# Kernel tuning notes

Hardware: AMD Instinct MI355X
Metric: run time of the kernel (lower is better)

The kernel has to match this reference:

```python
import jax, jax.numpy as jnp
import numpy as np

B, S, H, KVH, D = 2, 4096, 32, 8, 64
HID = H * D          # 2048
WIN = 256            # sliding window size (incl. self)
CHK = 128            # chunk size for linear attention
NREP = H // KVH


def setup_inputs() -> dict:
    key = jax.random.key(0)
    ks = jax.random.split(key, 5)
    hidden_states = jax.random.normal(ks[0], (B, S, HID), jnp.float32)
    # RoPE tables (Llama-style)
    inv_freq = 1.0 / (10000.0 ** (jnp.arange(0, D, 2, dtype=jnp.float32) / D))
    freqs = jnp.arange(S, dtype=jnp.float32)[:, None] * inv_freq[None, :]
    emb = jnp.concatenate([freqs, freqs], axis=-1)          # [S, D]
    cos = jnp.broadcast_to(jnp.cos(emb)[None], (B, S, D)).astype(jnp.float32)
    sin = jnp.broadcast_to(jnp.sin(emb)[None], (B, S, D)).astype(jnp.float32)
    scale = 0.02
    Wq = jax.random.normal(ks[1], (HID, HID), jnp.float32) * scale
    Wk = jax.random.normal(ks[2], (KVH * D, HID), jnp.float32) * scale
    Wv = jax.random.normal(ks[3], (KVH * D, HID), jnp.float32) * scale
    Wo = jax.random.normal(ks[4], (HID, HID), jnp.float32) * scale
    return {"hidden_states": hidden_states, "cos": cos, "sin": sin,
            "Wq": Wq, "Wk": Wk, "Wv": Wv, "Wo": Wo}


def rotate_half(x):
    x1, x2 = jnp.split(x, 2, axis=-1)
    return jnp.concatenate([-x2, x1], axis=-1)


def local_window_attention(q, k, v):
    nb = S // WIN
    qb = q.reshape(B, H, nb, WIN, D)
    kb = k.reshape(B, H, nb, WIN, D)
    vb = v.reshape(B, H, nb, WIN, D)
    zpad = jnp.zeros_like(kb[:, :, :1])
    kcat = jnp.concatenate([jnp.concatenate([zpad, kb[:, :, :-1]], axis=2), kb], axis=3)  # [B,H,nb,2W,D]
    vcat = jnp.concatenate([jnp.concatenate([zpad, vb[:, :, :-1]], axis=2), vb], axis=3)
    scores = jnp.einsum('bhnqd,bhnkd->bhnqk', qb, kcat) / jnp.sqrt(jnp.float32(D))
    i = jnp.arange(WIN)[:, None]          # query pos within block
    j = jnp.arange(2 * WIN)[None, :]      # key pos within concat window
    diff = i + WIN - j                    # q_abs - key_abs
    base = (diff >= 0) & (diff < WIN)     # causal + window
    n = jnp.arange(nb)[:, None, None]
    valid = (n * WIN + j[None] - WIN) >= 0   # key_abs >= 0 (mask block-0 padding)
    mask = base[None] & valid                # [nb, W, 2W]
    scores = jnp.where(mask[None, None], scores, -1e30)
    attn = jax.nn.softmax(scores, axis=-1)
    out = jnp.einsum('bhnqk,bhnkd->bhnqd', attn, vcat)
    return out.reshape(B, H, S, D)


def linear_memory_attention(q, k, v):
    # causal linear attention with elu+1 feature map, chunked prefix state
    phi = lambda x: jax.nn.elu(x) + 1.0
    nc = S // CHK
    pq = phi(q).reshape(B, H, nc, CHK, D)
    pk = phi(k).reshape(B, H, nc, CHK, D)
    vc = v.reshape(B, H, nc, CHK, D)
    # intra-chunk (causal within chunk)
    cm = jnp.tril(jnp.ones((CHK, CHK), bool))
    scores = jnp.einsum('bhncd,bhnkd->bhnck', pq, pk)
    scores = jnp.where(cm, scores, 0.0)
    num = jnp.einsum('bhnck,bhnkd->bhncd', scores, vc)
    den = scores.sum(-1)
    # inter-chunk via exclusive prefix sums of KV state
    kv = jnp.einsum('bhnkd,bhnke->bhnde', pk, vc)      # [B,H,nc,D,D]
    ks = pk.sum(axis=3)                                # [B,H,nc,D]
    z4 = jnp.zeros_like(kv[:, :, :1])
    Sprev = jnp.concatenate([z4, jnp.cumsum(kv, axis=2)[:, :, :-1]], axis=2)
    z3 = jnp.zeros_like(ks[:, :, :1])
    zprev = jnp.concatenate([z3, jnp.cumsum(ks, axis=2)[:, :, :-1]], axis=2)
    num = num + jnp.einsum('bhncd,bhnde->bhnce', pq, Sprev)
    den = den + jnp.einsum('bhncd,bhnd->bhnc', pq, zprev)
    out = num / (den[..., None] + 1e-6)
    return out.reshape(B, H, S, D)


def reference(hidden_states, cos, sin, Wq, Wk, Wv, Wo):
    q = jnp.einsum('bsh,oh->bso', hidden_states, Wq).reshape(B, S, H, D).transpose(0, 2, 1, 3)
    k = jnp.einsum('bsh,oh->bso', hidden_states, Wk).reshape(B, S, KVH, D).transpose(0, 2, 1, 3)
    v = jnp.einsum('bsh,oh->bso', hidden_states, Wv).reshape(B, S, KVH, D).transpose(0, 2, 1, 3)
    c = cos[:, None]  # [B,1,S,D]
    s = sin[:, None]
    q = q * c + rotate_half(q) * s
    k = k * c + rotate_half(k) * s
    k = jnp.repeat(k, NREP, axis=1)
    v = jnp.repeat(v, NREP, axis=1)
    local_out = local_window_attention(q, k, v)
    linear_out = linear_memory_attention(q, k, v)
    hybrid = 0.5 * local_out + 0.5 * linear_out              # [B,H,S,D]
    hybrid = hybrid.transpose(0, 2, 1, 3).reshape(B, S, HID)
    return jnp.einsum('bsh,oh->bso', hybrid, Wo)
```

## Files before the change

### kernel.cpp

```cpp
#include <hip/hip_runtime.h>

#define gB 2
#define gS 4096
#define gH 32
#define gKVH 8
#define gHID 2048
#define gNC 32
#define gBS (gB*gS)

using bf16x8 = __attribute__((ext_vector_type(8))) short;
using f32x4  = __attribute__((ext_vector_type(4))) float;

__device__ __forceinline__ float bf2f(unsigned short u){
  return __uint_as_float(((unsigned)u) << 16);
}
__device__ __forceinline__ unsigned short f2bf(float f){
  unsigned u = __float_as_uint(f);
  u = (u + 0x7fffu + ((u >> 16) & 1u)) >> 16;
  return (unsigned short)u;
}
__device__ __forceinline__ float phi_f(float x){ return x > 0.f ? x + 1.f : __expf(x); }

__device__ __forceinline__ void unpack8(uint4 v, unsigned short* o){
  o[0]=(unsigned short)(v.x&0xffffu); o[1]=(unsigned short)(v.x>>16);
  o[2]=(unsigned short)(v.y&0xffffu); o[3]=(unsigned short)(v.y>>16);
  o[4]=(unsigned short)(v.z&0xffffu); o[5]=(unsigned short)(v.z>>16);
  o[6]=(unsigned short)(v.w&0xffffu); o[7]=(unsigned short)(v.w>>16);
}
__device__ __forceinline__ uint4 pack8(const unsigned short* s){
  uint4 v;
  v.x = (unsigned)s[0] | ((unsigned)s[1]<<16);
  v.y = (unsigned)s[2] | ((unsigned)s[3]<<16);
  v.z = (unsigned)s[4] | ((unsigned)s[5]<<16);
  v.w = (unsigned)s[6] | ((unsigned)s[7]<<16);
  return v;
}

typedef const __attribute__((address_space(1))) void* gas_ptr;
typedef __attribute__((address_space(3))) void* las_ptr;
__device__ __forceinline__ void gload16(const void* g, void* l){
  __builtin_amdgcn_global_load_lds((gas_ptr)g, (las_ptr)l, 16, 0, 0);
}

__global__ void cvt_all(const float* __restrict__ hidden, const float* __restrict__ Wq,
                        const float* __restrict__ Wk, const float* __restrict__ Wv,
                        const float* __restrict__ Wo, unsigned short* __restrict__ hbf,
                        unsigned short* __restrict__ wqkv, unsigned short* __restrict__ wob)
{
  const long HG = (long)gBS*gHID/4;
  const long QG = 1048576, KG = 262144, VG = 262144, OG = 1048576;
  const long total = HG + QG + KG + VG + OG;
  long stride = (long)gridDim.x * blockDim.x;
  for (long i = (long)blockIdx.x*blockDim.x + threadIdx.x; i < total; i += stride){
    const float* src; unsigned short* dst; long off;
    if (i < HG)                { src = hidden; dst = hbf;                          off = i; }
    else if (i < HG+QG)        { src = Wq;     dst = wqkv;                         off = i - HG; }
    else if (i < HG+QG+KG)     { src = Wk;     dst = wqkv + (size_t)2048*gHID;     off = i - HG - QG; }
    else if (i < HG+QG+KG+VG)  { src = Wv;     dst = wqkv + (size_t)2560*gHID;     off = i - HG - QG - KG; }
    else                       { src = Wo;     dst = wob;                          off = i - HG - QG - KG - VG; }
    float4 v = *(const float4*)(src + off*4);
    ushort4 o;
    o.x = f2bf(v.x); o.y = f2bf(v.y); o.z = f2bf(v.z); o.w = f2bf(v.w);
    *(ushort4*)(dst + off*4) = o;
  }
}

__global__ __launch_bounds__(512, 2) void gemm_qkv(const unsigned short* __restrict__ A,
                                                   const unsigned short* __restrict__ Bm,
                                                   const float* __restrict__ cosb,
                                                   const float* __restrict__ sinb,
                                                   unsigned short* __restrict__ q_r,
                                                   unsigned short* __restrict__ k_r,
                                                   unsigned short* __restrict__ vproj)
{
  const int Kdim = 2048;
  __shared__ unsigned short Sh[2*24576];
  int tid = threadIdx.x, lane = tid & 63, w = tid >> 6, lr = lane & 15, lg = lane >> 4;
  int wm = w >> 2, wn = w & 3;
  const int ntn = 12;
  int nwg = gridDim.x;
  int bid = (int)blockIdx.x;
  int swz = (bid & 7) * (nwg >> 3) + (bid >> 3);
  long m0 = (long)(swz / ntn) * 128;
  long n0 = (long)(swz % ntn) * 256;
  const int NT = Kdim >> 6;

  f32x4 acc[4][4] = {};

  auto stage = [&](int t){
    int sbase = (t & 1) * 24576;
    int k0 = t << 6;
    #pragma unroll
    for (int i = 0; i < 2; ++i){
      int c = w*64 + lane + i*512;
      int row = c >> 3, g = c & 7;
      int colb = (g ^ (row & 7)) << 4;
      gload16((const char*)A + ((m0 + row) * (long)Kdim + k0) * 2 + colb,
              (void*)&Sh[sbase + (w*64 + i*512)*8]);
    }
    #pragma unroll
    for (int i = 0; i < 4; ++i){
      int c = w*64 + lane + i*512;
      int row = c >> 3, g = c & 7;
      int colb = (g ^ (row & 7)) << 4;
      gload16((const char*)Bm + ((n0 + row) * (long)Kdim + k0) * 2 + colb,
              (void*)&Sh[sbase + 8192 + (w*64 + i*512)*8]);
    }
  };

  stage(0);
  for (int t = 0; t < NT; ++t){
    asm volatile("s_waitcnt vmcnt(0)" ::: "memory");
    __builtin_amdgcn_s_barrier();
    if (t + 1 < NT) stage(t + 1);
    int sb = (t & 1) * 24576;
    #pragma unroll
    for (int kk = 0; kk < 2; ++kk){
      bf16x8 af[4], bfr[4];
      #pragma unroll
      for (int m = 0; m < 4; ++m){
        int row = wm*64 + m*16 + lr;
        af[m] = *(const bf16x8*)&Sh[sb + row*64 + (((kk*4 + lg) ^ (row & 7)) << 3)];
      }
      #pragma unroll
      for (int n = 0; n < 4; ++n){
        int row = wn*64 + n*16 + lr;
        bfr[n] = *(const bf16x8*)&Sh[sb + 8192 + row*64 + (((kk*4 + lg) ^ (row & 7)) << 3)];
      }
      __builtin_amdgcn_s_setprio(1);
      #pragma unroll
      for (int m = 0; m < 4; ++m)
        #pragma unroll
        for (int n = 0; n < 4; ++n)
          acc[m][n] = __builtin_amdgcn_mfma_f32_16x16x32_bf16(af[m], bfr[n], acc[m][n], 0, 0, 0);
      __builtin_amdgcn_s_setprio(0);
    }
  }

  long colbase = n0 + wn*64;
  if (colbase < 2048){
    int head = (int)(colbase >> 6);
    #pragma unroll
    for (int m = 0; m < 4; ++m)
      #pragma unroll
      for (int r = 0; r < 4; ++r){
        long srow = m0 + wm*64 + m*16 + 4*lg + r;
        int b = (int)(srow >> 12), s = (int)(srow & 4095);
        const float* cp = cosb + srow*64;
        const float* sp = sinb + srow*64;
        unsigned short* op = q_r + ((size_t)(b*gH + head)*gS + s)*64;
        #pragma unroll
        for (int n = 0; n < 2; ++n){
          int d = n*16 + lr;
          float x1 = acc[m][n][r], x2 = acc[m][n+2][r];
          op[d]      = f2bf(x1*cp[d]    - x2*sp[d]);
          op[d+32]   = f2bf(x2*cp[d+32] + x1*sp[d+32]);
        }
      }
  } else if (colbase < 2560){
    int head = (int)(colbase >> 6) - 32;
    #pragma unroll
    for (int m = 0; m < 4; ++m)
      #pragma unroll
      for (int r = 0; r < 4; ++r){
        long srow = m0 + wm*64 + m*16 + 4*lg + r;
        int b = (int)(srow >> 12), s = (int)(srow & 4095);
        const float* cp = cosb + srow*64;
        const float* sp = sinb + srow*64;
        unsigned short* op = k_r + ((size_t)(b*gKVH + head)*gS + s)*64;
        #pragma unroll
        for (int n = 0; n < 2; ++n){
          int d = n*16 + lr;
          float x1 = acc[m][n][r], x2 = acc[m][n+2][r];
          op[d]      = f2bf(x1*cp[d]    - x2*sp[d]);
          op[d+32]   = f2bf(x2*cp[d+32] + x1*sp[d+32]);
        }
      }
  } else {
    #pragma unroll
    for (int m = 0; m < 4; ++m)
      #pragma unroll
      for (int r = 0; r < 4; ++r){
        long srow = m0 + wm*64 + m*16 + 4*lg + r;
        unsigned short* op = vproj + (size_t)srow*512 + (colbase - 2560);
        #pragma unroll
        for (int n = 0; n < 4; ++n)
          op[n*16 + lr] = f2bf(acc[m][n][r]);
      }
  }
}

template<int OUT_BF16>
__global__ __launch_bounds__(512, 2) void gemm256(const unsigned short* __restrict__ A,
                                                  const unsigned short* __restrict__ Bm,
                                                  void* __restrict__ Cout,
                                                  int Mdim, int Ndim, int Kdim)
{
  __shared__ unsigned short Sh[2*32768];
  int tid = threadIdx.x, lane = tid & 63, w = tid >> 6, lr = lane & 15, lg = lane >> 4;
  int wm = w >> 2, wn = w & 3;
  int ntn = Ndim >> 8;
  int nwg = gridDim.x;
  int bid = (int)blockIdx.x;
  int swz = (bid & 7) * (nwg >> 3) + (bid >> 3);
  long m0 = (long)(swz / ntn) * 256;
  long n0 = (long)(swz % ntn) * 256;
  int NT = Kdim >> 6;

  f32x4 acc[8][4] = {};

  auto stage = [&](int t){
    int sbase = (t & 1) * 32768;
    int k0 = t << 6;
    #pragma unroll
    for (int i = 0; i < 4; ++i){
      int c = w*64 + lane + i*512;
      int row = c >> 3, g = c & 7;
      int colb = (g ^ (row & 7)) << 4;
      gload16((const char*)A + ((m0 + row) * (long)Kdim + k0) * 2 + colb,
              (void*)&Sh[sbase + (w*64 + i*512)*8]);
      gload16((const char*)Bm + ((n0 + row) * (long)Kdim + k0) * 2 + colb,
              (void*)&Sh[sbase + 16384 + (w*64 + i*512)*8]);
    }
  };

  stage(0);
  for (int t = 0; t < NT; ++t){
    asm volatile("s_waitcnt vmcnt(0)" ::: "memory");
    __builtin_amdgcn_s_barrier();
    if (t + 1 < NT) stage(t + 1);
    int sb = (t & 1) * 32768;
    #pragma unroll
    for (int kk = 0; kk < 2; ++kk){
      bf16x8 af[8], bfr[4];
      #pragma unroll
      for (int m = 0; m < 8; ++m){
        int row = wm*128 + m*16 + lr;
        af[m] = *(const bf16x8*)&Sh[sb + row*64 + (((kk*4 + lg) ^ (row & 7)) << 3)];
      }
      #pragma unroll
      for (int n = 0; n < 4; ++n){
        int row = wn*64 + n*16 + lr;
        bfr[n] = *(const bf16x8*)&Sh[sb + 16384 + row*64 + (((kk*4 + lg) ^ (row & 7)) << 3)];
      }
      __builtin_amdgcn_s_setprio(1);
      #pragma unroll
      for (int m = 0; m < 8; ++m)
        #pragma unroll
        for (int n = 0; n < 4; ++n)
          acc[m][n] = __builtin_amdgcn_mfma_f32_16x16x32_bf16(af[m], bfr[n], acc[m][n], 0, 0, 0);
      __builtin_amdgcn_s_setprio(0);
    }
  }

  #pragma unroll
  for (int m = 0; m < 8; ++m)
    #pragma unroll
    for (int n = 0; n < 4; ++n)
      #pragma unroll
      for (int r = 0; r < 4; ++r){
        long row = m0 + wm*128 + m*16 + 4*lg + r;
        long col = n0 + wn*64 + n*16 + lr;
        float v = acc[m][n][r];
        if (OUT_BF16) ((unsigned short*)Cout)[row*Ndim + col] = f2bf(v);
        else          ((float*)Cout)[row*Ndim + col] = v;
      }
}

__global__ __launch_bounds__(256) void transpose64(const unsigned short* __restrict__ in,
                                                   unsigned short* __restrict__ out,
                                                   int tokStride, int voff, int mode)
{
  __shared__ unsigned short T[64*72];
  int bid = blockIdx.x;
  int st = bid & 63; int kvh = (bid >> 6) & 7; int b = bid >> 9;
  int s0 = st*64;
  int tid = threadIdx.x;
  const unsigned short* ip;
  size_t tokstr;
  if (mode == 0){ ip = in + ((size_t)(b*gKVH+kvh)*gS + s0)*64;                  tokstr = 64; }
  else          { ip = in + (size_t)(b*gS+s0)*tokStride + voff + kvh*64;        tokstr = tokStride; }
  #pragma unroll
  for (int i = 0; i < 2; ++i){
    int cc = tid + 256*i; int sl = cc >> 3, ch = cc & 7;
    *(uint4*)&T[sl*72 + ch*8] = *(const uint4*)&ip[(size_t)sl*tokstr + ch*8];
  }
  __syncthreads();
  unsigned short* op = out + ((size_t)(b*gKVH+kvh)*64)*gS;
  #pragma unroll
  for (int i = 0; i < 2; ++i){
    int cc = tid + 256*i; int d = cc >> 3, ch = cc & 7;
    unsigned short t[8];
    #pragma unroll
    for (int u = 0; u < 8; ++u) t[u] = T[(ch*8+u)*72 + d];
    *(uint4*)&op[(size_t)d*gS + s0 + ch*8] = pack8(t);
  }
}

__global__ __launch_bounds__(512) void local_attn(const unsigned short* __restrict__ q_r,
                                                  const unsigned short* __restrict__ k_r,
                                                  const unsigned short* __restrict__ vt,
                                                  unsigned short* __restrict__ olocal)
{
  __shared__ unsigned short Qs[128*72];
  __shared__ unsigned short Ks[2][64*72];
  __shared__ unsigned short VTs[2][64*72];
  __shared__ unsigned short Ps[8*16*72];
  int bid = blockIdx.x;
  int qt = bid & 31; int h = (bid >> 5) & 31; int b = bid >> 10;
  int kvh = h >> 2;
  int q0 = qt*128;
  int tid = threadIdx.x, lane = tid & 63, w = tid >> 6, lr = lane & 15, lg = lane >> 4;
  const unsigned short* qp = q_r + ((size_t)(b*gH  +h  )*gS + q0)*64;
  const unsigned short* kp = k_r + ((size_t)(b*gKVH+kvh)*gS)*64;
  const unsigned short* vp = vt  + ((size_t)(b*gKVH+kvh)*64)*gS;

  #pragma unroll
  for (int i = 0; i < 2; ++i){
    int cc = tid + 512*i; int row = cc >> 3, ch = cc & 7;
    *(uint4*)&Qs[row*72 + ch*8] = *(const uint4*)&qp[row*64 + ch*8];
  }

  int kt0 = (q0 >= 256) ? 0 : ((256 - q0) >> 6);
  int krow = tid >> 3, kch = tid & 7;
  uint4 kreg, vreg;
  {
    int kb = q0 - 256 + kt0*64;
    kreg = *(const uint4*)&kp[(size_t)(kb+krow)*64 + kch*8];
    vreg = *(const uint4*)&vp[(size_t)krow*gS + kb + kch*8];
    *(uint4*)&Ks[0][krow*72 + kch*8]  = kreg;
    *(uint4*)&VTs[0][krow*72 + kch*8] = vreg;
  }

  float psum[4] = {0.f, 0.f, 0.f, 0.f};
  f32x4 accO[4] = {};
  int wq = w*16;

  for (int kt = kt0; kt < 6; ++kt){
    int cur = (kt - kt0) & 1;
    __syncthreads();
    bool more = (kt + 1 < 6);
    if (more){
      int kb2 = q0 - 256 + (kt+1)*64;
      kreg = *(const uint4*)&kp[(size_t)(kb2+krow)*64 + kch*8];
      vreg = *(const uint4*)&vp[(size_t)krow*gS + kb2 + kch*8];
    }

    f32x4 sc[4] = {};
    #pragma unroll
    for (int kk = 0; kk < 64; kk += 32){
      bf16x8 aq = *(const bf16x8*)&Qs[(wq+lr)*72 + kk + 8*lg];
      #pragma unroll
      for (int f = 0; f < 4; ++f){
        bf16x8 bk = *(const bf16x8*)&Ks[cur][(f*16+lr)*72 + kk + 8*lg];
        sc[f] = __builtin_amdgcn_mfma_f32_16x16x32_bf16(aq, bk, sc[f], 0, 0, 0);
      }
    }
    #pragma unroll
    for (int f = 0; f < 4; ++f)
      #pragma unroll
      for (int r = 0; r < 4; ++r){
        int i = wq + 4*lg + r;
        int j = kt*64 + f*16 + lr;
        bool keep = (j > i) && (j <= i + 256);
        float e = __expf(sc[f][r] * 0.125f);
        float p = keep ? e : 0.f;
        psum[r] += p;
        Ps[w*1152 + (4*lg + r)*72 + f*16 + lr] = f2bf(p);
      }
    #pragma unroll
    for (int kk = 0; kk < 64; kk += 32){
      bf16x8 ap = *(const bf16x8*)&Ps[w*1152 + lr*72 + kk + 8*lg];
      #pragma unroll
      for (int dt = 0; dt < 4; ++dt){
        bf16x8 bv = *(const bf16x8*)&VTs[cur][(dt*16+lr)*72 + kk + 8*lg];
        accO[dt] = __builtin_amdgcn_mfma_f32_16x16x32_bf16(ap, bv, accO[dt], 0, 0, 0);
      }
    }
    if (more){
      *(uint4*)&Ks[cur^1][krow*72 + kch*8]  = kreg;
      *(uint4*)&VTs[cur^1][krow*72 + kch*8] = vreg;
    }
  }
  #pragma unroll
  for (int off = 1; off < 16; off <<= 1)
    #pragma unroll
    for (int r = 0; r < 4; ++r) psum[r] += __shfl_xor(psum[r], off);
  #pragma unroll
  for (int dt = 0; dt < 4; ++dt)
    #pragma unroll
    for (int r = 0; r < 4; ++r){
      int s = q0 + wq + 4*lg + r;
      int d = dt*16 + lr;
      float o = accO[dt][r] / psum[r];
      olocal[((size_t)(b*gS+s)*gH + h)*64 + d] = f2bf(0.5f * o);
    }
}

__global__ __launch_bounds__(256) void lin_pass1(const unsigned short* __restrict__ ktr,
                                                 const unsigned short* __restrict__ vt,
                                                 float* __restrict__ kvbuf, float* __restrict__ ksbuf)
{
  __shared__ unsigned short pkT[64*136];
  __shared__ unsigned short vT[64*136];
  int bid = blockIdx.x;
  int c = bid & 31; int kvh = (bid >> 5) & 7; int b = bid >> 8;
  int tid = threadIdx.x, lane = tid & 63, w = tid >> 6, lr = lane & 15, lg = lane >> 4;
  int s0 = c*128;
  const unsigned short* kp = ktr + ((size_t)(b*gKVH+kvh)*64)*gS;
  const unsigned short* vp = vt  + ((size_t)(b*gKVH+kvh)*64)*gS;
  #pragma unroll
  for (int i = 0; i < 4; ++i){
    int cc = tid + 256*i; int d = cc >> 4, ch = cc & 15;
    unsigned short t[8]; unpack8(*(const uint4*)&kp[(size_t)d*gS + s0 + ch*8], t);
    #pragma unroll
    for (int u = 0; u < 8; ++u) t[u] = f2bf(phi_f(bf2f(t[u])));
    *(uint4*)&pkT[d*136 + ch*8] = pack8(t);
    *(uint4*)&vT[d*136 + ch*8]  = *(const uint4*)&vp[(size_t)d*gS + s0 + ch*8];
  }
  __syncthreads();
  f32x4 acc[4] = {};
  #pragma unroll
  for (int kk = 0; kk < 128; kk += 32){
    bf16x8 a = *(const bf16x8*)&pkT[(16*w+lr)*136 + kk + 8*lg];
    #pragma unroll
    for (int et = 0; et < 4; ++et){
      bf16x8 bv = *(const bf16x8*)&vT[(16*et+lr)*136 + kk + 8*lg];
      acc[et] = __builtin_amdgcn_mfma_f32_16x16x32_bf16(a, bv, acc[et], 0, 0, 0);
    }
  }
  size_t base = (size_t)((b*gKVH+kvh)*gNC + c);
  float* kvp = kvbuf + base*4096;
  #pragma unroll
  for (int et = 0; et < 4; ++et)
    #pragma unroll
    for (int r = 0; r < 4; ++r)
      kvp[(16*w + 4*lg + r)*64 + 16*et + lr] = acc[et][r];
  if (tid < 64){
    float sum = 0.f;
    for (int k = 0; k < 128; ++k) sum += bf2f(pkT[tid*136 + k]);
    ksbuf[base*64 + tid] = sum;
  }
}

__global__ void lin_pass2(float* __restrict__ kvbuf, float* __restrict__ ksbuf){
  int t = blockIdx.x*256 + threadIdx.x;
  const int per = 4096 + 64;
  if (t >= gB*gKVH*per) return;
  int bh = t / per; int e = t % per;
  if (e < 4096){
    float* p = kvbuf + (size_t)bh*gNC*4096 + e;
    float acc = 0.f;
    for (int cix = 0; cix < gNC; ++cix){ float v = p[(size_t)cix*4096]; p[(size_t)cix*4096] = acc; acc += v; }
  } else {
    float* p = ksbuf + (size_t)bh*gNC*64 + (e - 4096);
    float acc = 0.f;
    for (int cix = 0; cix < gNC; ++cix){ float v = p[cix*64]; p[cix*64] = acc; acc += v; }
  }
}

__global__ __launch_bounds__(256) void lin_pass3(const unsigned short* __restrict__ q_r,
                                                 const unsigned short* __restrict__ k_r,
                                                 const unsigned short* __restrict__ vt,
                                                 const float* __restrict__ Sprev,
                                                 const float* __restrict__ zprev,
                                                 const unsigned short* __restrict__ olocal,
                                                 unsigned short* __restrict__ hout)
{
  __shared__ unsigned short pq[128*72];
  __shared__ unsigned short pk[64*72];
  __shared__ unsigned short Ph[128*72];
  __shared__ unsigned short vT[64*72];
  __shared__ unsigned short SpT[64*72];
  __shared__ float zp[64];

  int bid = blockIdx.x;
  int c = bid & 31; int h = (bid >> 5) & 31; int b = bid >> 10;
  int kvh = h >> 2;
  int tid = threadIdx.x, lane = tid & 63, w = tid >> 6, lr = lane & 15, lg = lane >> 4;
  int s0 = c*128;
  const unsigned short* qp = q_r + ((size_t)(b*gH  +h  )*gS + s0)*64;
  const unsigned short* kp = k_r + ((size_t)(b*gKVH+kvh)*gS + s0)*64;
  const unsigned short* vp = vt  + ((size_t)(b*gKVH+kvh)*64)*gS;
  const float* Sp  = Sprev + ((size_t)((b*gKVH+kvh)*gNC + c))*4096;
  const float* zpg = zprev + ((size_t)((b*gKVH+kvh)*gNC + c))*64;

  #pragma unroll
  for (int i = 0; i < 4; ++i){
    int cc = tid + 256*i; int row = cc >> 3, d0 = (cc & 7)*8;
    unsigned short t[8]; unpack8(*(const uint4*)(qp + row*64 + d0), t);
    #pragma unroll
    for (int u = 0; u < 8; ++u) pq[row*72 + d0 + u] = f2bf(phi_f(bf2f(t[u])));
  }
  #pragma unroll
  for (int i = 0; i < 16; ++i){
    int f = tid + 256*i; int d = f >> 6, e = f & 63;
    SpT[e*72 + d] = f2bf(Sp[f]);
  }
  if (tid < 64) zp[tid] = zpg[tid];

  float den[2][4] = {};
  f32x4 accO[2][4] = {};

  for (int kh = 0; kh < 2; ++kh){
    __syncthreads();
    #pragma unroll
    for (int i = 0; i < 2; ++i){
      int cc = tid + 256*i; int kr = cc >> 3, d0 = (cc & 7)*8;
      unsigned short t[8]; unpack8(*(const uint4*)(kp + (kh*64+kr)*64 + d0), t);
      #pragma unroll
      for (int u = 0; u < 8; ++u) pk[kr*72 + d0 + u] = f2bf(phi_f(bf2f(t[u])));
      *(uint4*)&vT[kr*72 + d0] = *(const uint4*)&vp[(size_t)kr*gS + s0 + kh*64 + d0];
    }
    __syncthreads();

    f32x4 sc[2][4] = {};
    #pragma unroll
    for (int kk = 0; kk < 64; kk += 32){
      bf16x8 a[2];
      #pragma unroll
      for (int rt = 0; rt < 2; ++rt) a[rt] = *(const bf16x8*)&pq[(32*w+16*rt+lr)*72 + kk + 8*lg];
      #pragma unroll
      for (int ct = 0; ct < 4; ++ct){
        bf16x8 bk = *(const bf16x8*)&pk[(16*ct+lr)*72 + kk + 8*lg];
        #pragma unroll
        for (int rt = 0; rt < 2; ++rt)
          sc[rt][ct] = __builtin_amdgcn_mfma_f32_16x16x32_bf16(a[rt], bk, sc[rt][ct], 0, 0, 0);
      }
    }
    #pragma unroll
    for (int rt = 0; rt < 2; ++rt)
      #pragma unroll
      for (int ct = 0; ct < 4; ++ct)
        #pragma unroll
        for (int r = 0; r < 4; ++r){
          int qrow = 32*w + 16*rt + 4*lg + r;
          int krow = kh*64 + 16*ct + lr;
          float sv = (krow <= qrow) ? sc[rt][ct][r] : 0.f;
          den[rt][r] += sv;
          Ph[qrow*72 + 16*ct + lr] = f2bf(sv);
        }
    #pragma unroll
    for (int kk = 0; kk < 64; kk += 32){
      bf16x8 ap[2];
      #pragma unroll
      for (int rt = 0; rt < 2; ++rt) ap[rt] = *(const bf16x8*)&Ph[(32*w+16*rt+lr)*72 + kk + 8*lg];
      #pragma unroll
      for (int et = 0; et < 4; ++et){
        bf16x8 bv = *(const bf16x8*)&vT[(16*et+lr)*72 + kk + 8*lg];
        #pragma unroll
        for (int rt = 0; rt < 2; ++rt)
          accO[rt][et] = __builtin_amdgcn_mfma_f32_16x16x32_bf16(ap[rt], bv, accO[rt][et], 0, 0, 0);
      }
    }
  }
  #pragma unroll
  for (int kk = 0; kk < 64; kk += 32){
    bf16x8 a[2];
    #pragma unroll
    for (int rt = 0; rt < 2; ++rt) a[rt] = *(const bf16x8*)&pq[(32*w+16*rt+lr)*72 + kk + 8*lg];
    #pragma unroll
    for (int et = 0; et < 4; ++et){
      bf16x8 bs = *(const bf16x8*)&SpT[(16*et+lr)*72 + kk + 8*lg];
      #pragma unroll
      for (int rt = 0; rt < 2; ++rt)
        accO[rt][et] = __builtin_amdgcn_mfma_f32_16x16x32_bf16(a[rt], bs, accO[rt][et], 0, 0, 0);
    }
  }
  #pragma unroll
  for (int rt = 0; rt < 2; ++rt)
    #pragma unroll
    for (int r = 0; r < 4; ++r){
      int qrow = 32*w + 16*rt + 4*lg + r;
      float part = 0.f;
      #pragma unroll
      for (int u = 0; u < 4; ++u){
        int d = 4*lr + u;
        part += bf2f(pq[qrow*72 + d]) * zp[d];
      }
      den[rt][r] += part;
      #pragma unroll
      for (int off = 1; off < 16; off <<= 1)
        den[rt][r] += __shfl_xor(den[rt][r], off);
    }
  #pragma unroll
  for (int rt = 0; rt < 2; ++rt)
    #pragma unroll
    for (int et = 0; et < 4; ++et)
      #pragma unroll
      for (int r = 0; r < 4; ++r){
        int qrow = 32*w + 16*rt + 4*lg + r;
        int e = 16*et + lr;
        float o = accO[rt][et][r] / (den[rt][r] + 1e-6f);
        int s = s0 + qrow;
        size_t idx = ((size_t)(b*gS+s)*gH + h)*64 + e;
        hout[idx] = f2bf(bf2f(olocal[idx]) + 0.5f * o);
      }
}

extern "C" void kernel_launch(void* const* d_in, const int* in_sizes, int n_in,
                              void* d_out, int out_size, void* d_ws, size_t ws_size,
                              hipStream_t stream)
{
  const float* hidden = (const float*)d_in[0];
  const float* cosb   = (const float*)d_in[1];
  const float* sinb   = (const float*)d_in[2];
  const float* Wq     = (const float*)d_in[3];
  const float* Wk     = (const float*)d_in[4];
  const float* Wv     = (const float*)d_in[5];
  const float* Wo     = (const float*)d_in[6];
  float* out = (float*)d_out;

  char* ws = (char*)d_ws;
  size_t off = 0;
  auto alloc = [&](size_t bytes)->void*{
    void* p = ws + off; off += (bytes + 255) & ~(size_t)255; return p;
  };
  unsigned short* hbf    = (unsigned short*)alloc((size_t)gBS*gHID*2);
  unsigned short* wqkv   = (unsigned short*)alloc((size_t)3072*gHID*2);
  unsigned short* wob    = (unsigned short*)alloc((size_t)gHID*gHID*2);
  unsigned short* vproj  = (unsigned short*)alloc((size_t)gBS*512*2);
  unsigned short* q_r    = (unsigned short*)alloc((size_t)gBS*gHID*2);
  unsigned short* k_r    = (unsigned short*)alloc((size_t)gBS*512*2);
  unsigned short* ktr    = (unsigned short*)alloc((size_t)gBS*512*2);
  unsigned short* vt     = (unsigned short*)alloc((size_t)gBS*512*2);
  unsigned short* olocal = (unsigned short*)alloc((size_t)gBS*gHID*2);
  float* kvbuf           = (float*)alloc((size_t)gB*gKVH*gNC*4096*4);
  float* ksbuf           = (float*)alloc((size_t)gB*gKVH*gNC*64*4);

  cvt_all<<<dim3(2048), dim3(256), 0, stream>>>(hidden, Wq, Wk, Wv, Wo, hbf, wqkv, wob);

  gemm_qkv<<<dim3(64*12), dim3(512), 0, stream>>>(hbf, wqkv, cosb, sinb, q_r, k_r, vproj);

  transpose64<<<dim3(gB*gKVH*64), dim3(256), 0, stream>>>(k_r,   ktr, 64,  0, 0);
  transpose64<<<dim3(gB*gKVH*64), dim3(256), 0, stream>>>(vproj, vt,  512, 0, 1);

  local_attn<<<dim3(gB*gH*32), dim3(512), 0, stream>>>(q_r, k_r, vt, olocal);
  lin_pass1<<<dim3(gB*gKVH*gNC), dim3(256), 0, stream>>>(ktr, vt, kvbuf, ksbuf);
  lin_pass2<<<dim3((gB*gKVH*(4096+64) + 255)/256), dim3(256), 0, stream>>>(kvbuf, ksbuf);
  lin_pass3<<<dim3(gB*gH*gNC), dim3(256), 0, stream>>>(q_r, k_r, vt, kvbuf, ksbuf, olocal, hbf);

  gemm256<0><<<dim3(32*8), dim3(512), 0, stream>>>(hbf, wob, (void*)out, 8192, 2048, 2048);
}
```

Baseline: 329.7 us.

## Precompute GEMM load addresses, merge transposes, vectorize phi stores

Both GEMM kernels now compute their per-thread global source pointers and LDS destination offsets once before the K loop, so each stage only adds a K offset. The two transpose launches are merged into one kernel that picks K or V mode from the block index, removing one launch. In lin_pass3 the phi-transformed q and k values are packed and written to LDS as single 16-byte stores instead of eight scalar stores. Keeping the precomputed pointers alive adds register pressure in the GEMMs.

Result: no change. 328.7 us (-0.3%).

```diff
diff --git a/kernel.cpp b/kernel.cpp
--- a/kernel.cpp
+++ b/kernel.cpp
@@ -87,25 +87,29 @@
 
   f32x4 acc[4][4] = {};
 
+  const char* gsrc[6]; unsigned ldst[6];
+  #pragma unroll
+  for (int i = 0; i < 2; ++i){
+    int c = w*64 + lane + i*512;
+    int row = c >> 3, g = c & 7;
+    int colb = (g ^ (row & 7)) << 4;
+    gsrc[i] = (const char*)A + ((m0 + row) * (long)Kdim)*2 + colb;
+    ldst[i] = (unsigned)((w*64 + i*512)*16);
+  }
+  #pragma unroll
+  for (int i = 0; i < 4; ++i){
+    int c = w*64 + lane + i*512;
+    int row = c >> 3, g = c & 7;
+    int colb = (g ^ (row & 7)) << 4;
+    gsrc[2+i] = (const char*)Bm + ((n0 + row) * (long)Kdim)*2 + colb;
+    ldst[2+i] = (unsigned)(16384 + (w*64 + i*512)*16);
+  }
   auto stage = [&](int t){
-    int sbase = (t & 1) * 24576;
-    int k0 = t << 6;
-    #pragma unroll
-    for (int i = 0; i < 2; ++i){
-      int c = w*64 + lane + i*512;
-      int row = c >> 3, g = c & 7;
-      int colb = (g ^ (row & 7)) << 4;
-      gload16((const char*)A + ((m0 + row) * (long)Kdim + k0) * 2 + colb,
-              (void*)&Sh[sbase + (w*64 + i*512)*8]);
-    }
-    #pragma unroll
-    for (int i = 0; i < 4; ++i){
-      int c = w*64 + lane + i*512;
-      int row = c >> 3, g = c & 7;
-      int colb = (g ^ (row & 7)) << 4;
-      gload16((const char*)Bm + ((n0 + row) * (long)Kdim + k0) * 2 + colb,
-              (void*)&Sh[sbase + 8192 + (w*64 + i*512)*8]);
-    }
+    int sb = (t & 1) * 49152;
+    long kb = (long)t << 7;
+    #pragma unroll
+    for (int i = 0; i < 6; ++i)
+      gload16(gsrc[i] + kb, (char*)Sh + sb + ldst[i]);
   };
 
   stage(0);
@@ -209,19 +213,23 @@
 
   f32x4 acc[8][4] = {};
 
+  const char* gsrc[8]; unsigned ldst[8];
+  #pragma unroll
+  for (int i = 0; i < 4; ++i){
+    int c = w*64 + lane + i*512;
+    int row = c >> 3, g = c & 7;
+    int colb = (g ^ (row & 7)) << 4;
+    gsrc[i]   = (const char*)A  + ((m0 + row) * (long)Kdim)*2 + colb;
+    ldst[i]   = (unsigned)((w*64 + i*512)*16);
+    gsrc[4+i] = (const char*)Bm + ((n0 + row) * (long)Kdim)*2 + colb;
+    ldst[4+i] = (unsigned)(32768 + (w*64 + i*512)*16);
+  }
   auto stage = [&](int t){
-    int sbase = (t & 1) * 32768;
-    int k0 = t << 6;
-    #pragma unroll
-    for (int i = 0; i < 4; ++i){
-      int c = w*64 + lane + i*512;
-      int row = c >> 3, g = c & 7;
-      int colb = (g ^ (row & 7)) << 4;
-      gload16((const char*)A + ((m0 + row) * (long)Kdim + k0) * 2 + colb,
-              (void*)&Sh[sbase + (w*64 + i*512)*8]);
-      gload16((const char*)Bm + ((n0 + row) * (long)Kdim + k0) * 2 + colb,
-              (void*)&Sh[sbase + 16384 + (w*64 + i*512)*8]);
-    }
+    int sb = (t & 1) * 65536;
+    long kb = (long)t << 7;
+    #pragma unroll
+    for (int i = 0; i < 8; ++i)
+      gload16(gsrc[i] + kb, (char*)Sh + sb + ldst[i]);
   };
 
   stage(0);
@@ -267,19 +275,22 @@
       }
 }
 
-__global__ __launch_bounds__(256) void transpose64(const unsigned short* __restrict__ in,
-                                                   unsigned short* __restrict__ out,
-                                                   int tokStride, int voff, int mode)
+__global__ __launch_bounds__(256) void transpose2(const unsigned short* __restrict__ k_r,
+                                                  unsigned short* __restrict__ ktr,
+                                                  const unsigned short* __restrict__ vproj,
+                                                  unsigned short* __restrict__ vt)
 {
   __shared__ unsigned short T[64*72];
   int bid = blockIdx.x;
+  int mode = bid >> 10; bid &= 1023;
   int st = bid & 63; int kvh = (bid >> 6) & 7; int b = bid >> 9;
   int s0 = st*64;
   int tid = threadIdx.x;
   const unsigned short* ip;
+  unsigned short* out;
   size_t tokstr;
-  if (mode == 0){ ip = in + ((size_t)(b*gKVH+kvh)*gS + s0)*64;                  tokstr = 64; }
-  else          { ip = in + (size_t)(b*gS+s0)*tokStride + voff + kvh*64;        tokstr = tokStride; }
+  if (mode == 0){ ip = k_r + ((size_t)(b*gKVH+kvh)*gS + s0)*64;      out = ktr; tokstr = 64; }
+  else          { ip = vproj + (size_t)(b*gS+s0)*512 + kvh*64;       out = vt;  tokstr = 512; }
   #pragma unroll
   for (int i = 0; i < 2; ++i){
     int cc = tid + 256*i; int sl = cc >> 3, ch = cc & 7;
@@ -490,7 +501,8 @@
     int cc = tid + 256*i; int row = cc >> 3, d0 = (cc & 7)*8;
     unsigned short t[8]; unpack8(*(const uint4*)(qp + row*64 + d0), t);
     #pragma unroll
-    for (int u = 0; u < 8; ++u) pq[row*72 + d0 + u] = f2bf(phi_f(bf2f(t[u])));
+    for (int u = 0; u < 8; ++u) t[u] = f2bf(phi_f(bf2f(t[u])));
+    *(uint4*)&pq[row*72 + d0] = pack8(t);
   }
   #pragma unroll
   for (int i = 0; i < 16; ++i){
@@ -509,7 +521,8 @@
       int cc = tid + 256*i; int kr = cc >> 3, d0 = (cc & 7)*8;
       unsigned short t[8]; unpack8(*(const uint4*)(kp + (kh*64+kr)*64 + d0), t);
       #pragma unroll
-      for (int u = 0; u < 8; ++u) pk[kr*72 + d0 + u] = f2bf(phi_f(bf2f(t[u])));
+      for (int u = 0; u < 8; ++u) t[u] = f2bf(phi_f(bf2f(t[u])));
+      *(uint4*)&pk[kr*72 + d0] = pack8(t);
       *(uint4*)&vT[kr*72 + d0] = *(const uint4*)&vp[(size_t)kr*gS + s0 + kh*64 + d0];
     }
     __syncthreads();
@@ -632,8 +645,7 @@
 
   gemm_qkv<<<dim3(64*12), dim3(512), 0, stream>>>(hbf, wqkv, cosb, sinb, q_r, k_r, vproj);
 
-  transpose64<<<dim3(gB*gKVH*64), dim3(256), 0, stream>>>(k_r,   ktr, 64,  0, 0);
-  transpose64<<<dim3(gB*gKVH*64), dim3(256), 0, stream>>>(vproj, vt,  512, 0, 1);
+  transpose2<<<dim3(2048), dim3(256), 0, stream>>>(k_r, ktr, vproj, vt);
 
   local_attn<<<dim3(gB*gH*32), dim3(512), 0, stream>>>(q_r, k_r, vt, olocal);
   lin_pass1<<<dim3(gB*gKVH*gNC), dim3(256), 0, stream>>>(ktr, vt, kvbuf, ksbuf);
```
